# Kernel tuning notes

Measured on AMD Instinct MI355X. Metric: run time of the kernel, lower is better.

Reference implementation:

```python
import jax, jax.numpy as jnp
import numpy as np

B, N, C, H = 8, 784, 768, 16
HEAD_DIM = C // H
SCALE = HEAD_DIM ** -0.5


def rel_indices(num_patches):
    # ConViT relative position features: (dx, dy, dx^2+dy^2) per patch pair
    s = int(num_patches ** 0.5)
    ind = (jnp.arange(s)[None, :] - jnp.arange(s)[:, None]).astype(jnp.float32)
    indx = jnp.tile(ind, (s, s))                               # [N, N]
    indy = jnp.repeat(jnp.repeat(ind, s, axis=0), s, axis=1)   # [N, N]
    indd = indx ** 2 + indy ** 2
    return jnp.stack([indx, indy, indd], axis=-1)              # [N, N, 3]


def setup_inputs() -> dict:
    key = jax.random.key(0)
    ks = jax.random.split(key, 6)
    std = 0.02
    return {
        "x": jax.random.normal(ks[0], (B, N, C), dtype=jnp.float32),
        "Wq": jax.random.normal(ks[1], (C, C), dtype=jnp.float32) * std,
        "Wk": jax.random.normal(ks[2], (C, C), dtype=jnp.float32) * std,
        "Wv": jax.random.normal(ks[3], (C, C), dtype=jnp.float32) * std,
        "Wproj": jax.random.normal(ks[4], (C, C), dtype=jnp.float32) * std,
        "b_proj": jnp.zeros((C,), dtype=jnp.float32),
        "W_pos": jax.random.normal(ks[5], (H, 3), dtype=jnp.float32) * std,
        "b_pos": jnp.zeros((H,), dtype=jnp.float32),
        "gating": jnp.ones((H,), dtype=jnp.float32),
    }


def reference(x, Wq, Wk, Wv, Wproj, b_proj, W_pos, b_pos, gating):
    b, n, c = x.shape
    h, d = H, c // H

    def heads(W):
        # torch Linear: y = x @ W.T ; reshape to [b, h, n, d]
        return (x @ W.T).reshape(b, n, h, d).transpose(0, 2, 1, 3)

    q, k, v = heads(Wq), heads(Wk), heads(Wv)

    # content score: [b, h, n, n]
    patch_score = jnp.einsum('bhnd,bhmd->bhnm', q, k) * SCALE
    patch_score = jax.nn.softmax(patch_score, axis=-1)

    # positional score: rel [n,n,3] -> [h,n,n], broadcast over batch
    rel = rel_indices(n)
    pos_score = jnp.einsum('nmc,hc->hnm', rel, W_pos) + b_pos[:, None, None]
    pos_score = jax.nn.softmax(pos_score, axis=-1)

    g = jax.nn.sigmoid(gating)[None, :, None, None]  # [1,h,1,1]
    attn = (1.0 - g) * patch_score + g * pos_score[None]
    attn = attn / jnp.sum(attn, axis=-1, keepdims=True)

    out = jnp.einsum('bhnm,bhmd->bhnd', attn, v)
    out = out.transpose(0, 2, 1, 3).reshape(b, n, c)
    out = out @ Wproj.T + b_proj
    return out, attn, v
```

## Files before the change

kernel.cpp:

```cpp
#include <hip/hip_runtime.h>
#include <math.h>

#define BB 8
#define NN 784
#define CC 768
#define HH 16
#define DD 48
#define SCALE 0.14433756729740643f

#define ATTN_OFF ((size_t)BB*NN*CC)
#define V_OFF (ATTN_OFF + (size_t)BB*HH*NN*NN)

#define WS_XB ((size_t)0)
#define WS_WB ((size_t)4816896)
#define WS_QB (WS_WB + (size_t)4*589824)
#define WS_KB (WS_QB + (size_t)4816896)
#define WS_VT (WS_KB + (size_t)4816896)
#define WS_OB (WS_VT + (size_t)4816896)

using bf16x8 = __attribute__((ext_vector_type(8))) short;
using f32x4  = __attribute__((ext_vector_type(4))) float;

__device__ __forceinline__ short f2bf(float f) {
    union { float f; unsigned u; } uf; uf.f = f;
    unsigned u = uf.u;
    return (short)((u + 0x7FFFu + ((u >> 16) & 1u)) >> 16);
}
__device__ __forceinline__ bf16x8 bzero() {
    bf16x8 z = {0,0,0,0,0,0,0,0};
    return z;
}
__device__ __forceinline__ bf16x8 cvt8(float4 a, float4 b) {
    bf16x8 r;
    r[0]=f2bf(a.x); r[1]=f2bf(a.y); r[2]=f2bf(a.z); r[3]=f2bf(a.w);
    r[4]=f2bf(b.x); r[5]=f2bf(b.y); r[6]=f2bf(b.z); r[7]=f2bf(b.w);
    return r;
}
#define MFMA16(a,b,c) __builtin_amdgcn_mfma_f32_16x16x32_bf16((a),(b),(c),0,0,0)

__global__ __launch_bounds__(256) void cast_kernel(
    const float* __restrict__ x, const float* __restrict__ Wq,
    const float* __restrict__ Wk, const float* __restrict__ Wv,
    const float* __restrict__ Wp, short* __restrict__ xb, short* __restrict__ wb)
{
    int idx = blockIdx.x * 256 + threadIdx.x;
    const float* src;
    short* dst;
    if (idx < 1204224) {
        src = x + (size_t)idx * 4;
        dst = xb + (size_t)idx * 4;
    } else {
        int j = idx - 1204224;
        int sel = j / 147456;
        size_t off = (size_t)(j % 147456) * 4;
        const float* W = (sel == 0) ? Wq : (sel == 1) ? Wk : (sel == 2) ? Wv : Wp;
        src = W + off;
        dst = wb + (size_t)sel * 589824 + off;
    }
    float4 v = *(const float4*)src;
    union { short s[4]; uint2 u; } o;
    o.s[0] = f2bf(v.x); o.s[1] = f2bf(v.y); o.s[2] = f2bf(v.z); o.s[3] = f2bf(v.w);
    *(uint2*)dst = o.u;
}

__global__ __launch_bounds__(256) void qkv_mfma(
    const short* __restrict__ xb, const short* __restrict__ wb,
    short* __restrict__ qb, short* __restrict__ kb,
    float* __restrict__ vo, short* __restrict__ vt)
{
    const int t = threadIdx.x, l = t & 63, ww = t >> 6;
    const int quad = l >> 4, lc = l & 15;
    const int m0 = blockIdx.x * 128 + (ww >> 1) * 64;
    const int bn = blockIdx.y;
    const int wsel = bn / 6;
    const int colbase = (bn % 6) * 128 + (ww & 1) * 64;
    const short* W = wb + (size_t)wsel * 589824;

    f32x4 acc[4][4] = {};
    const short* arow = xb + (size_t)(m0 + lc) * 768 + quad * 8;
    const short* brow = W  + (size_t)(colbase + lc) * 768 + quad * 8;

    for (int k0 = 0; k0 < 768; k0 += 32) {
        bf16x8 af[4], bf[4];
#pragma unroll
        for (int i = 0; i < 4; i++) af[i] = *(const bf16x8*)(arow + (size_t)i * 16 * 768 + k0);
#pragma unroll
        for (int j = 0; j < 4; j++) bf[j] = *(const bf16x8*)(brow + (size_t)j * 16 * 768 + k0);
#pragma unroll
        for (int i = 0; i < 4; i++)
#pragma unroll
            for (int j = 0; j < 4; j++)
                acc[i][j] = MFMA16(af[i], bf[j], acc[i][j]);
    }

#pragma unroll
    for (int i = 0; i < 4; i++) {
#pragma unroll
        for (int j = 0; j < 4; j++) {
            const int o = colbase + j * 16 + lc;
            const int h = o / DD, d = o % DD;
#pragma unroll
            for (int r = 0; r < 4; r++) {
                const int m = m0 + i * 16 + quad * 4 + r;
                const int b = m / NN, n = m % NN;
                const size_t bhnd = (((size_t)b * HH + h) * NN + n) * DD + d;
                const float v = acc[i][j][r];
                if (wsel == 0)      qb[bhnd] = f2bf(v);
                else if (wsel == 1) kb[bhnd] = f2bf(v);
                else {
                    vo[bhnd] = v;
                    vt[((size_t)(b * HH + h) * DD + d) * NN + n] = f2bf(v);
                }
            }
        }
    }
}

__global__ __launch_bounds__(256) void attn_pv_fused(
    const short* __restrict__ qb, const short* __restrict__ kb,
    const short* __restrict__ vt,
    const float* __restrict__ W_pos, const float* __restrict__ b_pos,
    const float* __restrict__ gating, float* __restrict__ attn,
    short* __restrict__ ob)
{
    const int t = threadIdx.x, l = t & 63, ww = t >> 6;
    const int quad = l >> 4, lc = l & 15;
    const int bh = blockIdx.y, b = bh >> 4, h = bh & 15;
    const int row0 = blockIdx.x * 16;

    __shared__ float Sbuf[16][812];
    __shared__ float lxs[55], lys[55], fxs[55], fys[55];

    Sbuf[t >> 4][784 + (t & 15)] = 0.f;

    const short* qrow = qb + ((size_t)bh * NN + row0 + lc) * DD;
    bf16x8 qf0 = *(const bf16x8*)(qrow + quad * 8);
    bf16x8 qf1 = (quad < 2) ? *(const bf16x8*)(qrow + 32 + quad * 8) : bzero();

    for (int ct = ww; ct < 49; ct += 4) {
        const int c0 = ct * 16;
        const short* krow = kb + ((size_t)bh * NN + c0 + lc) * DD;
        bf16x8 kf0 = *(const bf16x8*)(krow + quad * 8);
        bf16x8 kf1 = (quad < 2) ? *(const bf16x8*)(krow + 32 + quad * 8) : bzero();
        f32x4 cc = {0.f, 0.f, 0.f, 0.f};
        cc = MFMA16(qf0, kf0, cc);
        cc = MFMA16(qf1, kf1, cc);
#pragma unroll
        for (int r = 0; r < 4; r++)
            Sbuf[quad * 4 + r][c0 + lc] = cc[r] * SCALE;
    }

    const float w0 = W_pos[h * 3], w1 = W_pos[h * 3 + 1], w2 = W_pos[h * 3 + 2];
    if (t < 55) {
        const float d = (float)(t - 27);
        lxs[t] = fmaf(w2, d * d, w0 * d);
    } else if (t >= 64 && t < 119) {
        const float d = (float)(t - 91);
        lys[t - 64] = fmaf(w2, d * d, w1 * d);
    }

    __syncthreads();

    if (t < 55) {
        float m = lxs[0];
#pragma unroll
        for (int i = 1; i < 55; i++) m = fmaxf(m, lxs[i]);
        fxs[t] = __expf(lxs[t] - m);
    } else if (t >= 64 && t < 119) {
        float m = lys[0];
#pragma unroll
        for (int i = 1; i < 55; i++) m = fmaxf(m, lys[i]);
        fys[t - 64] = __expf(lys[t - 64] - m);
    }

    const int r = t >> 4, c = t & 15;
    const int nrow = row0 + r;
    const int nx = nrow % 28, ny = nrow / 28;

    float sm = -1e30f;
#pragma unroll 7
    for (int s = 0; s < 49; s++) sm = fmaxf(sm, Sbuf[r][c + 16 * s]);
    sm = fmaxf(sm, __shfl_xor(sm, 1));
    sm = fmaxf(sm, __shfl_xor(sm, 2));
    sm = fmaxf(sm, __shfl_xor(sm, 4));
    sm = fmaxf(sm, __shfl_xor(sm, 8));
    float se = 0.f;
#pragma unroll 7
    for (int s = 0; s < 49; s++) {
        const float e = __expf(Sbuf[r][c + 16 * s] - sm);
        Sbuf[r][c + 16 * s] = e;
        se += e;
    }
    se += __shfl_xor(se, 1);
    se += __shfl_xor(se, 2);
    se += __shfl_xor(se, 4);
    se += __shfl_xor(se, 8);
    const float inv = 1.f / se;
    const float g = 1.f / (1.f + __expf(-gating[h]));

    __syncthreads();

    float Sx = 0.f, Sy = 0.f;
#pragma unroll
    for (int mx = 0; mx < 28; mx++) Sx += fxs[mx - nx + 27];
#pragma unroll
    for (int my = 0; my < 28; my++) Sy += fys[my - ny + 27];
    const float pinv = 1.f / (Sx * Sy);

    float sa = 0.f;
    {
        int mx = c, my = 0;
#pragma unroll 7
        for (int s = 0; s < 49; s++) {
            const int m = c + 16 * s;
            const float pos = fxs[mx - nx + 27] * fys[my - ny + 27] * pinv;
            const float a = (1.f - g) * Sbuf[r][m] * inv + g * pos;
            Sbuf[r][m] = a;
            sa += a;
            mx += 16;
            if (mx >= 28) { mx -= 28; my++; }
        }
    }
    sa += __shfl_xor(sa, 1);
    sa += __shfl_xor(sa, 2);
    sa += __shfl_xor(sa, 4);
    sa += __shfl_xor(sa, 8);
    const float inv2 = 1.f / sa;

    float* arow = attn + ((size_t)bh * NN + nrow) * NN;
#pragma unroll 7
    for (int s = 0; s < 49; s++) {
        const float val = Sbuf[r][c + 16 * s] * inv2;
        __builtin_nontemporal_store(val, arow + c + 16 * s);
        Sbuf[r][c + 16 * s] = val;
    }

    __syncthreads();

    if (ww < 3) {
        const short* vrow = vt + ((size_t)bh * DD + ww * 16 + lc) * NN;
        f32x4 acc = {0.f, 0.f, 0.f, 0.f};
        for (int kt = 0; kt < 25; kt++) {
            const int k0 = kt * 32 + quad * 8;
            bf16x8 af, bf;
            if (k0 < NN) {
                float4 a0 = *(const float4*)&Sbuf[lc][k0];
                float4 a1 = *(const float4*)&Sbuf[lc][k0 + 4];
                af = cvt8(a0, a1);
                bf = *(const bf16x8*)(vrow + k0);
            } else {
                af = bzero();
                bf = bzero();
            }
            acc = MFMA16(af, bf, acc);
        }
        const int d = h * DD + ww * 16 + lc;
#pragma unroll
        for (int rr = 0; rr < 4; rr++) {
            const int rowi = row0 + quad * 4 + rr;
            ob[((size_t)b * NN + rowi) * CC + d] = f2bf(acc[rr]);
        }
    }
}

__global__ __launch_bounds__(256) void proj_mfma(
    const short* __restrict__ ob, const short* __restrict__ wb,
    const float* __restrict__ bias, float* __restrict__ out)
{
    const int t = threadIdx.x, l = t & 63, ww = t >> 6;
    const int quad = l >> 4, lc = l & 15;
    const int m0 = blockIdx.x * 128 + (ww >> 1) * 64;
    const int colbase = blockIdx.y * 128 + (ww & 1) * 64;
    const short* W = wb + (size_t)3 * 589824;

    f32x4 acc[4][4] = {};
    const short* arow = ob + (size_t)(m0 + lc) * 768 + quad * 8;
    const short* brow = W  + (size_t)(colbase + lc) * 768 + quad * 8;

    for (int k0 = 0; k0 < 768; k0 += 32) {
        bf16x8 af[4], bf[4];
#pragma unroll
        for (int i = 0; i < 4; i++) af[i] = *(const bf16x8*)(arow + (size_t)i * 16 * 768 + k0);
#pragma unroll
        for (int j = 0; j < 4; j++) bf[j] = *(const bf16x8*)(brow + (size_t)j * 16 * 768 + k0);
#pragma unroll
        for (int i = 0; i < 4; i++)
#pragma unroll
            for (int j = 0; j < 4; j++)
                acc[i][j] = MFMA16(af[i], bf[j], acc[i][j]);
    }

#pragma unroll
    for (int i = 0; i < 4; i++) {
#pragma unroll
        for (int j = 0; j < 4; j++) {
            const int o = colbase + j * 16 + lc;
            const float bo = bias[o];
#pragma unroll
            for (int r = 0; r < 4; r++) {
                const int m = m0 + i * 16 + quad * 4 + r;
                out[(size_t)m * CC + o] = acc[i][j][r] + bo;
            }
        }
    }
}

extern "C" void kernel_launch(void* const* d_in, const int* in_sizes, int n_in,
                              void* d_out, int out_size, void* d_ws, size_t ws_size,
                              hipStream_t stream)
{
    const float* x      = (const float*)d_in[0];
    const float* Wq     = (const float*)d_in[1];
    const float* Wk     = (const float*)d_in[2];
    const float* Wv     = (const float*)d_in[3];
    const float* Wproj  = (const float*)d_in[4];
    const float* b_proj = (const float*)d_in[5];
    const float* W_pos  = (const float*)d_in[6];
    const float* b_pos  = (const float*)d_in[7];
    const float* gating = (const float*)d_in[8];

    float* out  = (float*)d_out;
    short* ws   = (short*)d_ws;

    short* xb = ws + WS_XB;
    short* wb = ws + WS_WB;
    short* qb = ws + WS_QB;
    short* kb = ws + WS_KB;
    short* vt = ws + WS_VT;
    short* ob = ws + WS_OB;
    float* attn = out + ATTN_OFF;
    float* vout = out + V_OFF;

    hipLaunchKernelGGL(cast_kernel, dim3(7008), dim3(256), 0, stream,
                       x, Wq, Wk, Wv, Wproj, xb, wb);
    hipLaunchKernelGGL(qkv_mfma, dim3(49, 18), dim3(256), 0, stream,
                       xb, wb, qb, kb, vout, vt);
    hipLaunchKernelGGL(attn_pv_fused, dim3(49, 128), dim3(256), 0, stream,
                       qb, kb, vt, W_pos, b_pos, gating, attn, ob);
    hipLaunchKernelGGL(proj_mfma, dim3(49, 6), dim3(256), 0, stream,
                       ob, wb, b_proj, out);
}
```

Measured before the change: 676.2 us.

## Fuse row-max into QK loop, drop renormalization pass, split PV over K

```diff
diff --git a/kernel.cpp b/kernel.cpp
--- a/kernel.cpp
+++ b/kernel.cpp
@@ -108,7 +108,7 @@
                 if (wsel == 0)      qb[bhnd] = f2bf(v);
                 else if (wsel == 1) kb[bhnd] = f2bf(v);
                 else {
-                    vo[bhnd] = v;
+                    __builtin_nontemporal_store(v, vo + bhnd);
                     vt[((size_t)(b * HH + h) * DD + d) * NN + n] = f2bf(v);
                 }
             }
@@ -128,8 +128,9 @@
     const int bh = blockIdx.y, b = bh >> 4, h = bh & 15;
     const int row0 = blockIdx.x * 16;
 
-    __shared__ float Sbuf[16][812];
+    __shared__ __align__(16) float Sbuf[16][812];
     __shared__ float lxs[55], lys[55], fxs[55], fys[55];
+    __shared__ float pmws[16][4];
 
     Sbuf[t >> 4][784 + (t & 15)] = 0.f;
 
@@ -137,17 +138,40 @@
     bf16x8 qf0 = *(const bf16x8*)(qrow + quad * 8);
     bf16x8 qf1 = (quad < 2) ? *(const bf16x8*)(qrow + 32 + quad * 8) : bzero();
 
-    for (int ct = ww; ct < 49; ct += 4) {
-        const int c0 = ct * 16;
-        const short* krow = kb + ((size_t)bh * NN + c0 + lc) * DD;
+    float pmax[4] = {-3e38f, -3e38f, -3e38f, -3e38f};
+    {
+        int ct = ww;
+        const short* krow = kb + ((size_t)bh * NN + ct * 16 + lc) * DD;
         bf16x8 kf0 = *(const bf16x8*)(krow + quad * 8);
         bf16x8 kf1 = (quad < 2) ? *(const bf16x8*)(krow + 32 + quad * 8) : bzero();
-        f32x4 cc = {0.f, 0.f, 0.f, 0.f};
-        cc = MFMA16(qf0, kf0, cc);
-        cc = MFMA16(qf1, kf1, cc);
-#pragma unroll
-        for (int r = 0; r < 4; r++)
-            Sbuf[quad * 4 + r][c0 + lc] = cc[r] * SCALE;
+        while (ct < 49) {
+            const int nct = ct + 4;
+            bf16x8 nk0 = bzero(), nk1 = bzero();
+            if (nct < 49) {
+                const short* nrow = kb + ((size_t)bh * NN + nct * 16 + lc) * DD;
+                nk0 = *(const bf16x8*)(nrow + quad * 8);
+                nk1 = (quad < 2) ? *(const bf16x8*)(nrow + 32 + quad * 8) : bzero();
+            }
+            f32x4 cc = {0.f, 0.f, 0.f, 0.f};
+            cc = MFMA16(qf0, kf0, cc);
+            cc = MFMA16(qf1, kf1, cc);
+            const int c0 = ct * 16;
+#pragma unroll
+            for (int r = 0; r < 4; r++) {
+                Sbuf[quad * 4 + r][c0 + lc] = cc[r] * SCALE;
+                pmax[r] = fmaxf(pmax[r], cc[r]);
+            }
+            kf0 = nk0; kf1 = nk1; ct = nct;
+        }
+    }
+#pragma unroll
+    for (int r = 0; r < 4; r++) {
+        float v = pmax[r];
+        v = fmaxf(v, __shfl_xor(v, 1));
+        v = fmaxf(v, __shfl_xor(v, 2));
+        v = fmaxf(v, __shfl_xor(v, 4));
+        v = fmaxf(v, __shfl_xor(v, 8));
+        if (lc == 0) pmws[quad * 4 + r][ww] = v;
     }
 
     const float w0 = W_pos[h * 3], w1 = W_pos[h * 3 + 1], w2 = W_pos[h * 3 + 2];
@@ -177,13 +201,8 @@
     const int nrow = row0 + r;
     const int nx = nrow % 28, ny = nrow / 28;
 
-    float sm = -1e30f;
-#pragma unroll 7
-    for (int s = 0; s < 49; s++) sm = fmaxf(sm, Sbuf[r][c + 16 * s]);
-    sm = fmaxf(sm, __shfl_xor(sm, 1));
-    sm = fmaxf(sm, __shfl_xor(sm, 2));
-    sm = fmaxf(sm, __shfl_xor(sm, 4));
-    sm = fmaxf(sm, __shfl_xor(sm, 8));
+    const float sm = SCALE * fmaxf(fmaxf(pmws[r][0], pmws[r][1]),
+                                   fmaxf(pmws[r][2], pmws[r][3]));
     float se = 0.f;
 #pragma unroll 7
     for (int s = 0; s < 49; s++) {
@@ -205,60 +224,69 @@
     for (int mx = 0; mx < 28; mx++) Sx += fxs[mx - nx + 27];
 #pragma unroll
     for (int my = 0; my < 28; my++) Sy += fys[my - ny + 27];
-    const float pinv = 1.f / (Sx * Sy);
-
-    float sa = 0.f;
+    const float ginv = (1.f - g) * inv;
+    const float gp = g / (Sx * Sy);
+
+    float* arow = attn + ((size_t)bh * NN + nrow) * NN;
     {
         int mx = c, my = 0;
 #pragma unroll 7
         for (int s = 0; s < 49; s++) {
             const int m = c + 16 * s;
-            const float pos = fxs[mx - nx + 27] * fys[my - ny + 27] * pinv;
-            const float a = (1.f - g) * Sbuf[r][m] * inv + g * pos;
+            const float a = fmaf(Sbuf[r][m], ginv,
+                                 fxs[mx - nx + 27] * fys[my - ny + 27] * gp);
             Sbuf[r][m] = a;
-            sa += a;
+            __builtin_nontemporal_store(a, arow + m);
             mx += 16;
             if (mx >= 28) { mx -= 28; my++; }
         }
     }
-    sa += __shfl_xor(sa, 1);
-    sa += __shfl_xor(sa, 2);
-    sa += __shfl_xor(sa, 4);
-    sa += __shfl_xor(sa, 8);
-    const float inv2 = 1.f / sa;
-
-    float* arow = attn + ((size_t)bh * NN + nrow) * NN;
-#pragma unroll 7
-    for (int s = 0; s < 49; s++) {
-        const float val = Sbuf[r][c + 16 * s] * inv2;
-        __builtin_nontemporal_store(val, arow + c + 16 * s);
-        Sbuf[r][c + 16 * s] = val;
-    }
-
-    __syncthreads();
-
-    if (ww < 3) {
-        const short* vrow = vt + ((size_t)bh * DD + ww * 16 + lc) * NN;
-        f32x4 acc = {0.f, 0.f, 0.f, 0.f};
-        for (int kt = 0; kt < 25; kt++) {
+
+    __syncthreads();
+
+    const short* vbase = vt + (size_t)bh * DD * NN;
+    f32x4 acc[3] = {};
+    {
+        const int kt0 = ww * 6;
+        const int kt1 = (ww == 3) ? 25 : kt0 + 6;
+        for (int kt = kt0; kt < kt1; kt++) {
             const int k0 = kt * 32 + quad * 8;
-            bf16x8 af, bf;
-            if (k0 < NN) {
-                float4 a0 = *(const float4*)&Sbuf[lc][k0];
-                float4 a1 = *(const float4*)&Sbuf[lc][k0 + 4];
-                af = cvt8(a0, a1);
-                bf = *(const bf16x8*)(vrow + k0);
-            } else {
-                af = bzero();
-                bf = bzero();
-            }
-            acc = MFMA16(af, bf, acc);
-        }
-        const int d = h * DD + ww * 16 + lc;
-#pragma unroll
-        for (int rr = 0; rr < 4; rr++) {
-            const int rowi = row0 + quad * 4 + rr;
-            ob[((size_t)b * NN + rowi) * CC + d] = f2bf(acc[rr]);
+            float4 a0 = *(const float4*)&Sbuf[lc][k0];
+            float4 a1 = *(const float4*)&Sbuf[lc][k0 + 4];
+            bf16x8 af = cvt8(a0, a1);
+#pragma unroll
+            for (int j = 0; j < 3; j++) {
+                bf16x8 bf = (k0 < NN)
+                    ? *(const bf16x8*)(vbase + (size_t)(j * 16 + lc) * NN + k0)
+                    : bzero();
+                acc[j] = MFMA16(af, bf, acc[j]);
+            }
+        }
+    }
+
+    __syncthreads();
+
+    float* Pacc = &Sbuf[0][0];
+    if (ww > 0) {
+#pragma unroll
+        for (int j = 0; j < 3; j++)
+            *(f32x4*)&Pacc[(((ww - 1) * 3 + j) * 64 + l) * 4] = acc[j];
+    }
+
+    __syncthreads();
+
+    if (ww == 0) {
+#pragma unroll
+        for (int j = 0; j < 3; j++) {
+#pragma unroll
+            for (int w = 0; w < 3; w++)
+                acc[j] += *(const f32x4*)&Pacc[((w * 3 + j) * 64 + l) * 4];
+            const int d = h * DD + j * 16 + lc;
+#pragma unroll
+            for (int rr = 0; rr < 4; rr++) {
+                const int rowi = row0 + quad * 4 + rr;
+                ob[((size_t)b * NN + rowi) * CC + d] = f2bf(acc[j][rr]);
+            }
         }
     }
 }
@@ -299,7 +327,7 @@
 #pragma unroll
             for (int r = 0; r < 4; r++) {
                 const int m = m0 + i * 16 + quad * 4 + r;
-                out[(size_t)m * CC + o] = acc[i][j][r] + bo;
+                __builtin_nontemporal_store(acc[i][j][r] + bo, out + (size_t)m * CC + o);
             }
         }
     }
```

New measurement: 638.3 us. -5.6%, faster.
